# Kernel optimization log

Measured on AMD Instinct MI355X. Metric: run time of the kernel, lower is better.

Reference implementation:

```python
import jax, jax.numpy as jnp
import numpy as np

MAX_NUM_BINS = 200
BIN_SIZE = 500
NUM_NEIGHBORS = 5
DIST_MULT = 0.1


def setup_inputs() -> dict:
    key = jax.random.key(0)
    k1, k2 = jax.random.split(key)
    points = jax.random.normal(k1, (2, 5000, 128), dtype=jnp.float32)
    rotations = jax.random.normal(k2, (128, MAX_NUM_BINS // 2), dtype=jnp.float32)
    return {"points": points, "rotations": rotations}


def reference(points, rotations):
    # points: [B, N, D], rotations: [D, max_num_bins//2]
    B, N, D = points.shape
    nbins = N // BIN_SIZE  # module requires N % BIN_SIZE == 0

    # LSH bin assignment: project onto nbins//2 random directions, sign-split into nbins bins
    mul = jnp.einsum('bnd,dh->bnh', points, rotations[:, :nbins // 2])  # [B,N,nbins//2]
    cmul = jnp.concatenate([mul, -mul], axis=-1)                        # [B,N,nbins]
    bin_idx = jnp.argmax(cmul, axis=-1)                                 # [B,N]
    # equal-size bins via argsort of bin id (matches tf argsort+reshape)
    bins_split = jnp.argsort(bin_idx, axis=-1).reshape(B, nbins, BIN_SIZE)  # [B,nbins,S]

    # gather points per bin
    parts = jnp.take_along_axis(points, bins_split.reshape(B, N, 1), axis=1)
    parts = parts.reshape(B, nbins, BIN_SIZE, D)

    # per-bin pairwise distance -> gaussian kernel
    na = jnp.sum(parts * parts, axis=-1)                                # [B,nbins,S]
    gram = jnp.einsum('bcid,bcjd->bcij', parts, parts)                  # [B,nbins,S,S]
    dist = jnp.sqrt(jnp.maximum(na[..., :, None] - 2.0 * gram + na[..., None, :], 1e-6))
    dm = jnp.exp(-DIST_MULT * dist)                                     # [B,nbins,S,S]

    # top-k neighbors within each bin
    vals, idx = jax.lax.top_k(dm, NUM_NEIGHBORS)                        # [B,nbins,S,K]

    # map local bin indices back to global point indices
    bs_flat = bins_split.reshape(B * nbins, BIN_SIZE)
    dst = jnp.take_along_axis(bs_flat, idx.reshape(B * nbins, BIN_SIZE * NUM_NEIGHBORS), axis=1)
    dst = dst.reshape(B, nbins, BIN_SIZE, NUM_NEIGHBORS)
    src = jnp.broadcast_to(bins_split[..., None], dst.shape)
    bidx = jnp.broadcast_to(jnp.arange(B)[:, None, None, None], dst.shape)

    # scatter-add into dense [B,N,N] (sparse.add sums duplicate entries)
    out = jnp.zeros((B, N, N), dtype=points.dtype)
    out = out.at[bidx.reshape(-1), src.reshape(-1), dst.reshape(-1)].add(vals.reshape(-1))
    return out
```

## Files before the change

### kernel.cpp

```cpp
#include <hip/hip_runtime.h>
#include <cfloat>
#include <math.h>

#define NPTS   5000
#define BATCH  2
#define DIM    128
#define NBINS  10
#define BINSZ  500
#define TOPK   5
#define ROTCOLS 100

#define KB_PTS 64
#define KB_STR 129
__global__ void k_bins(const float* __restrict__ pts, const float* __restrict__ rot,
                       int* __restrict__ bin_idx, double* __restrict__ na) {
    __shared__ float P[KB_PTS * KB_STR];
    __shared__ float rotL[DIM * 5];
    int tid = threadIdx.x;
    for (int f = tid; f < DIM * 5; f += 256)
        rotL[f] = rot[(f / 5) * ROTCOLS + (f % 5)];

    int p0  = blockIdx.x * KB_PTS;
    int npb = min(KB_PTS, BATCH * NPTS - p0);

    for (int f = tid; f < npb * DIM; f += 256) {
        int r = f >> 7, d = f & 127;
        P[r * KB_STR + d] = pts[(size_t)(p0 + r) * DIM + d];
    }
    __syncthreads();

    int p = tid >> 2;
    int s = tid & 3;
    double acc[5] = {0., 0., 0., 0., 0.};
    double sq = 0.;
    const float* row = &P[p * KB_STR + s * 32];
    for (int j = 0; j < 32; ++j) {
        double v = (double)row[j];
        sq += v * v;
        int d = s * 32 + j;
#pragma unroll
        for (int h = 0; h < 5; ++h) acc[h] += v * (double)rotL[d * 5 + h];
    }
#pragma unroll
    for (int m = 1; m < 4; m <<= 1) {
#pragma unroll
        for (int h = 0; h < 5; ++h) acc[h] += __shfl_xor(acc[h], m, 4);
        sq += __shfl_xor(sq, m, 4);
    }
    if (s == 0 && p < npb) {
        double best = acc[0]; int bc = 0;
#pragma unroll
        for (int c = 1; c < NBINS; ++c) {
            double v = (c < 5) ? acc[c] : -acc[c - 5];
            if (v > best) { best = v; bc = c; }
        }
        bin_idx[p0 + p] = bc;
        na[p0 + p] = sq;
    }
}

__global__ void k_sort(const int* __restrict__ bin_idx, int* __restrict__ order) {
    const int b = blockIdx.x;
    const int t = threadIdx.x;
    const int NPT = (NPTS + 255) / 256;
    int start = t * NPT;
    int end   = min(NPTS, start + NPT);

    int cnt[NBINS];
#pragma unroll
    for (int c = 0; c < NBINS; ++c) cnt[c] = 0;
    for (int i = start; i < end; ++i) {
        int c = bin_idx[b * NPTS + i];
#pragma unroll
        for (int k = 0; k < NBINS; ++k) cnt[k] += (c == k);
    }

    __shared__ int hist[NBINS * 256];
#pragma unroll
    for (int c = 0; c < NBINS; ++c) hist[c * 256 + t] = cnt[c];
    __syncthreads();

    int base = t * NBINS;
    int s = 0;
#pragma unroll
    for (int k = 0; k < NBINS; ++k) s += hist[base + k];
    __shared__ int scan[256];
    scan[t] = s;
    __syncthreads();
    for (int off = 1; off < 256; off <<= 1) {
        int v = (t >= off) ? scan[t - off] : 0;
        __syncthreads();
        scan[t] += v;
        __syncthreads();
    }
    int run = scan[t] - s;
#pragma unroll
    for (int k = 0; k < NBINS; ++k) { int h = hist[base + k]; hist[base + k] = run; run += h; }
    __syncthreads();

    int ofs[NBINS];
#pragma unroll
    for (int c = 0; c < NBINS; ++c) ofs[c] = hist[c * 256 + t];
    for (int i = start; i < end; ++i) {
        int c = bin_idx[b * NPTS + i];
        int pos = 0;
#pragma unroll
        for (int k = 0; k < NBINS; ++k) {
            if (c == k) pos = ofs[k];
            ofs[k] += (c == k);
        }
        order[b * NPTS + pos] = i;
    }
}

#define RT    16
#define NRT   32
#define CTILE 64
#define RSTRD 130
#define CSTR  132
#define NCT   8
#define ROWQ  (NPTS/4)

__launch_bounds__(256, 3)
__global__ void k_chunks(const float* __restrict__ pts, const double* __restrict__ na,
                         const int* __restrict__ order, float* __restrict__ out) {
    __shared__ double rowPd[RT * RSTRD];
    __shared__ float  colP[CTILE * CSTR];
    __shared__ double naC[CTILE];
    __shared__ double naRs[RT];
    __shared__ int    ordR[RT];

    int blk   = blockIdx.x;
    int rt    = blk & (NRT - 1);
    int chunk = blk >> 5;
    int b     = chunk / NBINS;
    int c     = chunk % NBINS;
    int tid   = threadIdx.x;
    int row0  = rt * RT;
    int rowCount = min(RT, BINSZ - row0);

    const int*   ordBase = order + b * NPTS + c * BINSZ;
    const float* ptsB    = pts + (size_t)b * NPTS * DIM;

    for (int f = tid; f < rowCount * (DIM / 4); f += 256) {
        int r = f >> 5;
        int q = f & 31;
        int g = ordBase[row0 + r];
        float4 v = *(const float4*)(ptsB + (size_t)g * DIM + q * 4);
        double2 d01; d01.x = (double)v.x; d01.y = (double)v.y;
        double2 d23; d23.x = (double)v.z; d23.y = (double)v.w;
        *(double2*)(&rowPd[r * RSTRD + q * 4 + 0]) = d01;
        *(double2*)(&rowPd[r * RSTRD + q * 4 + 2]) = d23;
    }
    if (tid < rowCount) {
        int g = ordBase[row0 + tid];
        ordR[tid] = g;
        naRs[tid] = na[b * NPTS + g];
    }
    __syncthreads();

    int rg = tid >> 5;
    int cg = tid & 31;

    double naRr0 = (rg     < rowCount) ? naRs[rg]     : 0.;
    double naRr1 = (rg + 8 < rowCount) ? naRs[rg + 8] : 0.;

    double tv[2][TOPK];
    int    tl[2][TOPK];
#pragma unroll
    for (int ii = 0; ii < 2; ++ii)
#pragma unroll
        for (int k = 0; k < TOPK; ++k) { tv[ii][k] = DBL_MAX; tl[ii][k] = 0x7fffffff; }

    const int totalZ = rowCount * ROWQ;

    for (int ct = 0; ct < NCT; ++ct) {
        int col0 = ct * CTILE;
        int colCount = min(CTILE, BINSZ - col0);
        __syncthreads();
        for (int f = tid; f < colCount * (DIM / 4); f += 256) {
            int j = f >> 5;
            int q = f & 31;
            int g = ordBase[col0 + j];
            float4 v = *(const float4*)(ptsB + (size_t)g * DIM + q * 4);
            *(float4*)(&colP[j * CSTR + q * 4]) = v;
        }
        if (tid < colCount) {
            int g = ordBase[col0 + tid];
            naC[tid] = na[b * NPTS + g];
        }
        __syncthreads();

        {
            float4 z = make_float4(0.f, 0.f, 0.f, 0.f);
            int z0 = (ct * totalZ) / NCT, z1 = ((ct + 1) * totalZ) / NCT;
            for (int f = z0 + tid; f < z1; f += 256) {
                int r = f / ROWQ;
                int q = f - r * ROWQ;
                float* outRow = out + ((size_t)b * NPTS + ordR[r]) * NPTS;
                *(float4*)(outRow + 4 * q) = z;
            }
        }

        double acc00 = 0., acc01 = 0., acc10 = 0., acc11 = 0.;

        for (int q = 0; q < DIM / 4; ++q) {
            double2 a0lo = *(const double2*)(&rowPd[rg * RSTRD + q * 4 + 0]);
            double2 a0hi = *(const double2*)(&rowPd[rg * RSTRD + q * 4 + 2]);
            double2 a1lo = *(const double2*)(&rowPd[(rg + 8) * RSTRD + q * 4 + 0]);
            double2 a1hi = *(const double2*)(&rowPd[(rg + 8) * RSTRD + q * 4 + 2]);
            float4 b0 = *(const float4*)(&colP[cg * CSTR + q * 4]);
            float4 b1 = *(const float4*)(&colP[(cg + 32) * CSTR + q * 4]);
            double b00 = (double)b0.x, b01 = (double)b0.y,
                   b02 = (double)b0.z, b03 = (double)b0.w;
            double b10 = (double)b1.x, b11 = (double)b1.y,
                   b12 = (double)b1.z, b13 = (double)b1.w;
            acc00 += a0lo.x * b00 + a0lo.y * b01 + a0hi.x * b02 + a0hi.y * b03;
            acc01 += a0lo.x * b10 + a0lo.y * b11 + a0hi.x * b12 + a0hi.y * b13;
            acc10 += a1lo.x * b00 + a1lo.y * b01 + a1hi.x * b02 + a1hi.y * b03;
            acc11 += a1lo.x * b10 + a1lo.y * b11 + a1hi.x * b12 + a1hi.y * b13;
        }

#pragma unroll
        for (int jj = 0; jj < 2; ++jj) {
            int j = cg + 32 * jj;
            if (j < colCount) {
                int    cl = col0 + j;
                double nc = naC[j];
                double a0 = (jj == 0) ? acc00 : acc01;
                double a1 = (jj == 0) ? acc10 : acc11;
                double cv0 = fmax(naRr0 + nc - 2. * a0, 1e-6);
                double cv1 = fmax(naRr1 + nc - 2. * a1, 1e-6);
                int cl0 = cl, cl1 = cl;
#pragma unroll
                for (int k = 0; k < TOPK; ++k) {
                    bool lt0 = (cv0 < tv[0][k]);
                    double ov0 = tv[0][k]; int ol0 = tl[0][k];
                    if (lt0) { tv[0][k] = cv0; tl[0][k] = cl0; cv0 = ov0; cl0 = ol0; }
                    bool lt1 = (cv1 < tv[1][k]);
                    double ov1 = tv[1][k]; int ol1 = tl[1][k];
                    if (lt1) { tv[1][k] = cv1; tl[1][k] = cl1; cv1 = ov1; cl1 = ol1; }
                }
            }
        }
    }

#pragma unroll
    for (int m = 1; m < 32; m <<= 1) {
#pragma unroll
        for (int ii = 0; ii < 2; ++ii) {
            double rv[TOPK]; int rl[TOPK];
#pragma unroll
            for (int k = 0; k < TOPK; ++k) {
                rv[k] = __shfl_xor(tv[ii][k], m, 32);
                rl[k] = __shfl_xor(tl[ii][k], m, 32);
            }
#pragma unroll
            for (int k = 0; k < TOPK; ++k) {
                double cv = rv[k]; int cl = rl[k];
#pragma unroll
                for (int s = 0; s < TOPK; ++s) {
                    bool better = (cv < tv[ii][s]) || (cv == tv[ii][s] && cl < tl[ii][s]);
                    double ov = tv[ii][s]; int ol = tl[ii][s];
                    if (better) { tv[ii][s] = cv; tl[ii][s] = cl; cv = ov; cl = ol; }
                }
            }
        }
    }

    __syncthreads();

    if (cg == 0) {
#pragma unroll
        for (int ii = 0; ii < 2; ++ii) {
            int r = rg + 8 * ii;
            if (r < rowCount) {
                int src = ordR[r];
                float* outRow = out + ((size_t)b * NPTS + src) * NPTS;
#pragma unroll
                for (int k = 0; k < TOPK; ++k) {
                    double dist = sqrt(tv[ii][k]);
                    double dm   = exp(-0.1 * dist);
                    int dst = ordBase[tl[ii][k]];
                    outRow[dst] = (float)dm;
                }
            }
        }
    }
}

extern "C" void kernel_launch(void* const* d_in, const int* in_sizes, int n_in,
                              void* d_out, int out_size, void* d_ws, size_t ws_size,
                              hipStream_t stream) {
    const float* pts = (const float*)d_in[0];
    const float* rot = (const float*)d_in[1];
    float* out = (float*)d_out;

    double* na      = (double*)d_ws;
    int*    bin_idx = (int*)((char*)d_ws + 80000);
    int*    order   = (int*)((char*)d_ws + 120000);

    k_bins<<<(BATCH * NPTS + KB_PTS - 1) / KB_PTS, 256, 0, stream>>>(pts, rot, bin_idx, na);
    k_sort<<<BATCH, 256, 0, stream>>>(bin_idx, order);
    k_chunks<<<BATCH * NBINS * NRT, 256, 0, stream>>>(pts, na, order, out);
}
```

Baseline: 296.3 us.

## Split column tiles across blocks and merge partial top-k in a separate kernel

Each block now handles one 16-row by 64-column tile instead of looping over all eight column tiles. This raises the grid from 640 to 5120 blocks, exposing more parallelism for the FP64 Gram computation and the output zeroing. Each block writes its partial top-5 keys and indices to workspace. A new k_merge kernel reduces the eight partials per row and writes the final exp(-0.1*sqrt) values. The cost is reloading row tiles eight times, an extra kernel launch, and a few MB of workspace traffic.

```diff
diff --git a/kernel.cpp b/kernel.cpp
--- a/kernel.cpp
+++ b/kernel.cpp
@@ -116,14 +116,15 @@
 #define RT    16
 #define NRT   32
 #define CTILE 64
+#define NCTL  8
 #define RSTRD 130
 #define CSTR  132
-#define NCT   8
 #define ROWQ  (NPTS/4)
 
 __launch_bounds__(256, 3)
-__global__ void k_chunks(const float* __restrict__ pts, const double* __restrict__ na,
-                         const int* __restrict__ order, float* __restrict__ out) {
+__global__ void k_gram(const float* __restrict__ pts, const double* __restrict__ na,
+                       const int* __restrict__ order, double* __restrict__ ckey,
+                       int* __restrict__ clid, float* __restrict__ out) {
     __shared__ double rowPd[RT * RSTRD];
     __shared__ float  colP[CTILE * CSTR];
     __shared__ double naC[CTILE];
@@ -131,13 +132,16 @@
     __shared__ int    ordR[RT];
 
     int blk   = blockIdx.x;
-    int rt    = blk & (NRT - 1);
-    int chunk = blk >> 5;
+    int ctile = blk & 7;
+    int rtile = (blk >> 3) & 31;
+    int chunk = blk >> 8;
     int b     = chunk / NBINS;
     int c     = chunk % NBINS;
     int tid   = threadIdx.x;
-    int row0  = rt * RT;
+    int row0  = rtile * RT;
+    int col0  = ctile * CTILE;
     int rowCount = min(RT, BINSZ - row0);
+    int colCount = min(CTILE, BINSZ - col0);
 
     const int*   ordBase = order + b * NPTS + c * BINSZ;
     const float* ptsB    = pts + (size_t)b * NPTS * DIM;
@@ -152,12 +156,35 @@
         *(double2*)(&rowPd[r * RSTRD + q * 4 + 0]) = d01;
         *(double2*)(&rowPd[r * RSTRD + q * 4 + 2]) = d23;
     }
+    for (int f = tid; f < colCount * (DIM / 4); f += 256) {
+        int j = f >> 5;
+        int q = f & 31;
+        int g = ordBase[col0 + j];
+        float4 v = *(const float4*)(ptsB + (size_t)g * DIM + q * 4);
+        *(float4*)(&colP[j * CSTR + q * 4]) = v;
+    }
     if (tid < rowCount) {
         int g = ordBase[row0 + tid];
         ordR[tid] = g;
         naRs[tid] = na[b * NPTS + g];
     }
-    __syncthreads();
+    if (tid < colCount) {
+        int g = ordBase[col0 + tid];
+        naC[tid] = na[b * NPTS + g];
+    }
+    __syncthreads();
+
+    {
+        float4 z = make_float4(0.f, 0.f, 0.f, 0.f);
+        int total = rowCount * ROWQ;
+        int z0 = (ctile * total) / NCTL, z1 = ((ctile + 1) * total) / NCTL;
+        for (int f = z0 + tid; f < z1; f += 256) {
+            int r = f / ROWQ;
+            int q = f - r * ROWQ;
+            float* outRow = out + ((size_t)b * NPTS + ordR[r]) * NPTS;
+            *(float4*)(outRow + 4 * q) = z;
+        }
+    }
 
     int rg = tid >> 5;
     int cg = tid & 31;
@@ -172,75 +199,43 @@
 #pragma unroll
         for (int k = 0; k < TOPK; ++k) { tv[ii][k] = DBL_MAX; tl[ii][k] = 0x7fffffff; }
 
-    const int totalZ = rowCount * ROWQ;
-
-    for (int ct = 0; ct < NCT; ++ct) {
-        int col0 = ct * CTILE;
-        int colCount = min(CTILE, BINSZ - col0);
-        __syncthreads();
-        for (int f = tid; f < colCount * (DIM / 4); f += 256) {
-            int j = f >> 5;
-            int q = f & 31;
-            int g = ordBase[col0 + j];
-            float4 v = *(const float4*)(ptsB + (size_t)g * DIM + q * 4);
-            *(float4*)(&colP[j * CSTR + q * 4]) = v;
-        }
-        if (tid < colCount) {
-            int g = ordBase[col0 + tid];
-            naC[tid] = na[b * NPTS + g];
-        }
-        __syncthreads();
-
-        {
-            float4 z = make_float4(0.f, 0.f, 0.f, 0.f);
-            int z0 = (ct * totalZ) / NCT, z1 = ((ct + 1) * totalZ) / NCT;
-            for (int f = z0 + tid; f < z1; f += 256) {
-                int r = f / ROWQ;
-                int q = f - r * ROWQ;
-                float* outRow = out + ((size_t)b * NPTS + ordR[r]) * NPTS;
-                *(float4*)(outRow + 4 * q) = z;
-            }
-        }
-
-        double acc00 = 0., acc01 = 0., acc10 = 0., acc11 = 0.;
-
-        for (int q = 0; q < DIM / 4; ++q) {
-            double2 a0lo = *(const double2*)(&rowPd[rg * RSTRD + q * 4 + 0]);
-            double2 a0hi = *(const double2*)(&rowPd[rg * RSTRD + q * 4 + 2]);
-            double2 a1lo = *(const double2*)(&rowPd[(rg + 8) * RSTRD + q * 4 + 0]);
-            double2 a1hi = *(const double2*)(&rowPd[(rg + 8) * RSTRD + q * 4 + 2]);
-            float4 b0 = *(const float4*)(&colP[cg * CSTR + q * 4]);
-            float4 b1 = *(const float4*)(&colP[(cg + 32) * CSTR + q * 4]);
-            double b00 = (double)b0.x, b01 = (double)b0.y,
-                   b02 = (double)b0.z, b03 = (double)b0.w;
-            double b10 = (double)b1.x, b11 = (double)b1.y,
-                   b12 = (double)b1.z, b13 = (double)b1.w;
-            acc00 += a0lo.x * b00 + a0lo.y * b01 + a0hi.x * b02 + a0hi.y * b03;
-            acc01 += a0lo.x * b10 + a0lo.y * b11 + a0hi.x * b12 + a0hi.y * b13;
-            acc10 += a1lo.x * b00 + a1lo.y * b01 + a1hi.x * b02 + a1hi.y * b03;
-            acc11 += a1lo.x * b10 + a1lo.y * b11 + a1hi.x * b12 + a1hi.y * b13;
-        }
-
-#pragma unroll
-        for (int jj = 0; jj < 2; ++jj) {
-            int j = cg + 32 * jj;
-            if (j < colCount) {
-                int    cl = col0 + j;
-                double nc = naC[j];
-                double a0 = (jj == 0) ? acc00 : acc01;
-                double a1 = (jj == 0) ? acc10 : acc11;
-                double cv0 = fmax(naRr0 + nc - 2. * a0, 1e-6);
-                double cv1 = fmax(naRr1 + nc - 2. * a1, 1e-6);
-                int cl0 = cl, cl1 = cl;
-#pragma unroll
-                for (int k = 0; k < TOPK; ++k) {
-                    bool lt0 = (cv0 < tv[0][k]);
-                    double ov0 = tv[0][k]; int ol0 = tl[0][k];
-                    if (lt0) { tv[0][k] = cv0; tl[0][k] = cl0; cv0 = ov0; cl0 = ol0; }
-                    bool lt1 = (cv1 < tv[1][k]);
-                    double ov1 = tv[1][k]; int ol1 = tl[1][k];
-                    if (lt1) { tv[1][k] = cv1; tl[1][k] = cl1; cv1 = ov1; cl1 = ol1; }
-                }
+    double acc00 = 0., acc01 = 0., acc10 = 0., acc11 = 0.;
+    for (int q = 0; q < DIM / 4; ++q) {
+        double2 a0lo = *(const double2*)(&rowPd[rg * RSTRD + q * 4 + 0]);
+        double2 a0hi = *(const double2*)(&rowPd[rg * RSTRD + q * 4 + 2]);
+        double2 a1lo = *(const double2*)(&rowPd[(rg + 8) * RSTRD + q * 4 + 0]);
+        double2 a1hi = *(const double2*)(&rowPd[(rg + 8) * RSTRD + q * 4 + 2]);
+        float4 b0 = *(const float4*)(&colP[cg * CSTR + q * 4]);
+        float4 b1 = *(const float4*)(&colP[(cg + 32) * CSTR + q * 4]);
+        double b00 = (double)b0.x, b01 = (double)b0.y,
+               b02 = (double)b0.z, b03 = (double)b0.w;
+        double b10 = (double)b1.x, b11 = (double)b1.y,
+               b12 = (double)b1.z, b13 = (double)b1.w;
+        acc00 += a0lo.x * b00 + a0lo.y * b01 + a0hi.x * b02 + a0hi.y * b03;
+        acc01 += a0lo.x * b10 + a0lo.y * b11 + a0hi.x * b12 + a0hi.y * b13;
+        acc10 += a1lo.x * b00 + a1lo.y * b01 + a1hi.x * b02 + a1hi.y * b03;
+        acc11 += a1lo.x * b10 + a1lo.y * b11 + a1hi.x * b12 + a1hi.y * b13;
+    }
+
+#pragma unroll
+    for (int jj = 0; jj < 2; ++jj) {
+        int j = cg + 32 * jj;
+        if (j < colCount) {
+            int    cl = col0 + j;
+            double nc = naC[j];
+            double a0 = (jj == 0) ? acc00 : acc01;
+            double a1 = (jj == 0) ? acc10 : acc11;
+            double cv0 = fmax(naRr0 + nc - 2. * a0, 1e-6);
+            double cv1 = fmax(naRr1 + nc - 2. * a1, 1e-6);
+            int cl0 = cl, cl1 = cl;
+#pragma unroll
+            for (int k = 0; k < TOPK; ++k) {
+                bool lt0 = (cv0 < tv[0][k]);
+                double ov0 = tv[0][k]; int ol0 = tl[0][k];
+                if (lt0) { tv[0][k] = cv0; tl[0][k] = cl0; cv0 = ov0; cl0 = ol0; }
+                bool lt1 = (cv1 < tv[1][k]);
+                double ov1 = tv[1][k]; int ol1 = tl[1][k];
+                if (lt1) { tv[1][k] = cv1; tl[1][k] = cl1; cv1 = ov1; cl1 = ol1; }
             }
         }
     }
@@ -268,24 +263,53 @@
         }
     }
 
-    __syncthreads();
-
     if (cg == 0) {
 #pragma unroll
         for (int ii = 0; ii < 2; ++ii) {
             int r = rg + 8 * ii;
             if (r < rowCount) {
-                int src = ordR[r];
-                float* outRow = out + ((size_t)b * NPTS + src) * NPTS;
+                int rowIdx = b * NPTS + c * BINSZ + row0 + r;
+                int base = rowIdx * (NCTL * TOPK) + ctile * TOPK;
 #pragma unroll
                 for (int k = 0; k < TOPK; ++k) {
-                    double dist = sqrt(tv[ii][k]);
-                    double dm   = exp(-0.1 * dist);
-                    int dst = ordBase[tl[ii][k]];
-                    outRow[dst] = (float)dm;
+                    ckey[base + k] = tv[ii][k];
+                    clid[base + k] = tl[ii][k];
                 }
             }
         }
+    }
+}
+
+__global__ void k_merge(const int* __restrict__ order, const double* __restrict__ ckey,
+                        const int* __restrict__ clid, float* __restrict__ out) {
+    int row = blockIdx.x * 256 + threadIdx.x;
+    if (row >= BATCH * NPTS) return;
+    int b    = row / NPTS;
+    int binb = row - (row % BINSZ);
+    int src  = order[row];
+
+    double bv[TOPK]; int bl[TOPK];
+#pragma unroll
+    for (int k = 0; k < TOPK; ++k) { bv[k] = DBL_MAX; bl[k] = 0x7fffffff; }
+
+    const double* kp = ckey + (size_t)row * (NCTL * TOPK);
+    const int*    lp = clid + (size_t)row * (NCTL * TOPK);
+    for (int m = 0; m < NCTL * TOPK; ++m) {
+        double cv = kp[m];
+        int    cl = lp[m];
+#pragma unroll
+        for (int k = 0; k < TOPK; ++k) {
+            bool better = (cv < bv[k]) || (cv == bv[k] && cl < bl[k]);
+            double ov = bv[k]; int ol = bl[k];
+            if (better) { bv[k] = cv; bl[k] = cl; cv = ov; cl = ol; }
+        }
+    }
+
+    float* outRow = out + ((size_t)b * NPTS + src) * NPTS;
+#pragma unroll
+    for (int k = 0; k < TOPK; ++k) {
+        int dst = order[binb + bl[k]];
+        outRow[dst] = (float)exp(-0.1 * sqrt(bv[k]));
     }
 }
 
@@ -299,8 +323,11 @@
     double* na      = (double*)d_ws;
     int*    bin_idx = (int*)((char*)d_ws + 80000);
     int*    order   = (int*)((char*)d_ws + 120000);
+    double* ckey    = (double*)((char*)d_ws + 160000);
+    int*    clid    = (int*)((char*)d_ws + 160000 + 3200000);
 
     k_bins<<<(BATCH * NPTS + KB_PTS - 1) / KB_PTS, 256, 0, stream>>>(pts, rot, bin_idx, na);
     k_sort<<<BATCH, 256, 0, stream>>>(bin_idx, order);
-    k_chunks<<<BATCH * NBINS * NRT, 256, 0, stream>>>(pts, na, order, out);
-}
+    k_gram<<<BATCH * NBINS * NRT * NCTL, 256, 0, stream>>>(pts, na, order, ckey, clid, out);
+    k_merge<<<(BATCH * NPTS + 255) / 256, 256, 0, stream>>>(order, ckey, clid, out);
+}
```

Measured after the change: 386.8 us. 1.31x slower.
